# Performance work log

Hardware: AMD Instinct MI355X
Metric: run time of the kernel (lower is better)

## Reference

```python
import jax, jax.numpy as jnp
import numpy as np

N_SERIES = 1024  # N; x carries 3N stacked time-synchronous nodes
GCN_DEPTH = 2
IN_DIM = 64
H_DIM = 64


def setup_inputs() -> dict:
    key = jax.random.key(0)
    k = jax.random.split(key, 6)
    B, C, N3 = 64, IN_DIM, 3 * N_SERIES
    x = jax.random.normal(k[0], (N3, B, C), dtype=jnp.float32)
    A = jax.random.normal(k[1], (N3, N3), dtype=jnp.float32) * 0.02
    # Linear2d (1x1 conv) params per depth; act='glu' -> out = 2*h_dim
    s0 = 1.0 / np.sqrt(IN_DIM)
    s1 = 1.0 / np.sqrt(H_DIM)
    W0 = jax.random.uniform(k[2], (2 * H_DIM, IN_DIM), jnp.float32, -s0, s0)
    b0 = jax.random.uniform(k[3], (2 * H_DIM,), jnp.float32, -s0, s0)
    W1 = jax.random.uniform(k[4], (2 * H_DIM, H_DIM), jnp.float32, -s1, s1)
    b1 = jax.random.uniform(k[5], (2 * H_DIM,), jnp.float32, -s1, s1)
    return {"x": x, "A": A, "W0": W0, "b0": b0, "W1": W1, "b1": b1}


def reference(x, A, W0, b0, W1, b1):
    # x: (3N, B, C) -> (B, C, 3N)
    h = jnp.transpose(x, (1, 2, 0))
    convs = []
    for W, b in ((W0, b0), (W1, b1)):
        # GCN2d flow='tgt_to_src': h[b,c,v] = sum_w h[b,c,w] * A[v,w]  (L=1 squeezed)
        g = jnp.einsum('bcw,vw->bcv', h, A)
        # Linear2d 1x1 conv: channels C -> 2*h_dim, then GLU gate
        y = jnp.einsum('oc,bcv->bov', W, g) + b[None, :, None]
        lhs, rhs = jnp.split(y, 2, axis=1)
        h = lhs * jax.nn.sigmoid(rhs)          # (B, h_dim, 3N)
        convs.append(jnp.transpose(h, (2, 0, 1)))  # (3N, B, h_dim)
    # crop the middle N nodes of each depth, then max over depth
    cropped = jnp.stack([c[N_SERIES:2 * N_SERIES] for c in convs], axis=0)
    return jnp.max(cropped, axis=0)  # (N, B, h_dim)
```

## Files before the change

kernel.cpp:

```cpp
#include <hip/hip_runtime.h>
#include <hip/hip_bf16.h>
#include <stdint.h>

typedef __attribute__((ext_vector_type(8))) short s16x8;
typedef __attribute__((ext_vector_type(4))) float f32x4;
typedef __attribute__((ext_vector_type(8))) unsigned short u16x8;
typedef __attribute__((ext_vector_type(4))) unsigned short u16x4;

__device__ __forceinline__ float bf2f(unsigned short u) {
  union { uint32_t u; float f; } v; v.u = ((uint32_t)u) << 16; return v.f;
}
__device__ __forceinline__ unsigned short f2bf(float f) {
  union { float f; uint32_t u; } v; v.f = f;
  uint32_t u = v.u;
  return (unsigned short)((u + 0x7fffu + ((u >> 16) & 1u)) >> 16);
}
__device__ __forceinline__ void load_lds16(const void* g, void* l) {
  __builtin_amdgcn_global_load_lds(
      (const __attribute__((address_space(1))) void*)g,
      (__attribute__((address_space(3))) void*)l, 16, 0, 0);
}

template <int N>
__device__ __forceinline__ void vmw() {
  if constexpr (N == 0) asm volatile("s_waitcnt vmcnt(0)" ::: "memory");
  else if constexpr (N == 1) asm volatile("s_waitcnt vmcnt(1)" ::: "memory");
  else if constexpr (N == 2) asm volatile("s_waitcnt vmcnt(2)" ::: "memory");
  else if constexpr (N == 3) asm volatile("s_waitcnt vmcnt(3)" ::: "memory");
  else if constexpr (N == 4) asm volatile("s_waitcnt vmcnt(4)" ::: "memory");
  else if constexpr (N == 5) asm volatile("s_waitcnt vmcnt(5)" ::: "memory");
  else if constexpr (N == 6) asm volatile("s_waitcnt vmcnt(6)" ::: "memory");
  else if constexpr (N == 7) asm volatile("s_waitcnt vmcnt(7)" ::: "memory");
  else asm volatile("s_waitcnt vmcnt(8)" ::: "memory");
}
#define SBAR() asm volatile("s_barrier" ::: "memory")

__global__ __launch_bounds__(256) void k_prep(const void* __restrict__ xin,
                                              const void* __restrict__ Ain,
                                              const void* __restrict__ W0,
                                              const void* __restrict__ b0,
                                              const void* __restrict__ W1,
                                              const void* __restrict__ b1,
                                              unsigned short* __restrict__ xtp,
                                              unsigned short* __restrict__ Abp,
                                              unsigned short* __restrict__ wb) {
  __shared__ __align__(16) unsigned short sh[64 * 65];
  const int t = threadIdx.x;
  const int bid = blockIdx.x;
  int fp;
  {
    uint32_t u = ((const uint32_t*)xin)[(t & 63) * 97 + 1];
    int e = (u >> 7) & 0xFF;
    unsigned long long m = __ballot(e > 150);
    fp = (__popcll(m) > 6) ? 1 : 0;
  }

  if (bid < 3072) {
    const int w0 = (bid % 48) * 64;
    const int m0 = (bid / 48) * 64;
    if (fp) {
      const float* xf = (const float*)xin;
#pragma unroll
      for (int rep = 0; rep < 4; ++rep) {
        int vi = t + rep * 256;
        int r = vi >> 4;
        int c4 = (vi & 15) * 4;
        f32x4 v = *(const f32x4*)(xf + (uint64_t)(w0 + r) * 4096 + m0 + c4);
#pragma unroll
        for (int u = 0; u < 4; ++u) sh[(c4 + u) * 65 + r] = f2bf(v[u]);
      }
    } else {
      const unsigned short* xb = (const unsigned short*)xin;
#pragma unroll
      for (int rep = 0; rep < 2; ++rep) {
        int vi = t + rep * 256;
        int r = vi >> 3;
        int c8 = (vi & 7) * 8;
        u16x8 v = *(const u16x8*)(xb + (uint64_t)(w0 + r) * 4096 + m0 + c8);
#pragma unroll
        for (int u = 0; u < 8; ++u) sh[(c8 + u) * 65 + r] = v[u];
      }
    }
    __syncthreads();
    unsigned short* dst = xtp + ((uint64_t)(m0 >> 6) * 48 + (w0 >> 6)) * 4096;
#pragma unroll
    for (int rep = 0; rep < 2; ++rep) {
      int vi = t + rep * 256;
      int kb = vi >> 6, r = vi & 63;
      u16x8 v;
#pragma unroll
      for (int u = 0; u < 8; ++u) v[u] = sh[r * 65 + kb * 8 + u];
      *(u16x8*)(dst + kb * 512 + r * 8) = v;
    }
  } else if (bid < 5376) {
    const int b2 = bid - 3072;
    const int kt = b2 % 48, rt = b2 / 48;
    if (fp) {
      const float* Af = (const float*)Ain;
#pragma unroll
      for (int rep = 0; rep < 4; ++rep) {
        int vi = t + rep * 256;
        int r = vi >> 4;
        int c4 = (vi & 15) * 4;
        f32x4 v = *(const f32x4*)(Af + (uint64_t)(rt * 64 + r) * 3072 + kt * 64 + c4);
        int kb = c4 >> 3, e = c4 & 7;
#pragma unroll
        for (int u = 0; u < 4; ++u) sh[kb * 520 + r * 8 + e + u] = f2bf(v[u]);
      }
    } else {
      const unsigned short* Ab16 = (const unsigned short*)Ain;
#pragma unroll
      for (int rep = 0; rep < 2; ++rep) {
        int vi = t + rep * 256;
        int r = vi >> 3;
        int c8 = (vi & 7) * 8;
        u16x8 v = *(const u16x8*)(Ab16 + (uint64_t)(rt * 64 + r) * 3072 + kt * 64 + c8);
#pragma unroll
        for (int u = 0; u < 8; ++u) sh[(c8 >> 3) * 520 + r * 8 + u] = v[u];
      }
    }
    __syncthreads();
    unsigned short* dst = Abp + ((uint64_t)rt * 48 + kt) * 4096;
#pragma unroll
    for (int rep = 0; rep < 2; ++rep) {
      int vi = t + rep * 256;
      int kb = vi >> 6, r = vi & 63;
      u16x8 v;
#pragma unroll
      for (int u = 0; u < 8; ++u) v[u] = sh[kb * 520 + r * 8 + u];
      *(u16x8*)(dst + kb * 512 + r * 8) = v;
    }
  } else {
    for (int i = t; i < 16640; i += 256) {
      const void* src; int off;
      if (i < 8192)        { src = W0; off = i; }
      else if (i < 8320)   { src = b0; off = i - 8192; }
      else if (i < 16512)  { src = W1; off = i - 8320; }
      else                 { src = b1; off = i - 16512; }
      wb[i] = fp ? f2bf(((const float*)src)[off]) : ((const unsigned short*)src)[off];
    }
  }
}

__global__ __launch_bounds__(512, 2) void k1_gemm_glu(
    const unsigned short* __restrict__ Am,
    const unsigned short* __restrict__ Bm,
    const unsigned short* __restrict__ W,
    const unsigned short* __restrict__ bias,
    unsigned short* __restrict__ H) {
  constexpr int BM  = 192;
  constexpr int IF  = 6;
  constexpr int IPH = 3;
  constexpr int APL = 12;
  constexpr int P   = 28;
  constexpr int QF  = 3;
  constexpr int PPW = 4;
  constexpr int BUFS = P * 512;
  constexpr int NT  = 96;
  constexpr int Kt  = 48;
  constexpr int NRB = 12;
  constexpr int SME = 4 * BUFS;

  __shared__ __align__(16) unsigned short smem[SME];

  const int t    = threadIdx.x;
  const int lane = t & 63;
  const int wid  = t >> 6;
  const int wV   = wid >> 2;
  const int wM   = wid & 3;
  const int fr   = lane & 15;
  const int q4   = lane >> 4;
  const int v0   = blockIdx.x * BM;
  const int m0   = blockIdx.y * 256;
  const int art0 = v0 >> 6;
  const int brt0 = m0 >> 6;

  const int myq = QF + ((wid < 4) ? 1 : 0);
  const unsigned short* srcb[PPW];
  int ldso[PPW];
#pragma unroll
  for (int q = 0; q < PPW; ++q) {
    int pi = wid + 8 * q;
    if (pi >= P) pi = P - 1;
    const int isA = pi < APL;
    const int rtl = (isA ? pi : pi - APL) >> 2;
    const int pb  = pi & 3;
    const unsigned short* base =
        isA ? (Am + (uint64_t)(art0 + rtl) * Kt * 4096)
            : (Bm + (uint64_t)(brt0 + rtl) * Kt * 4096);
    srcb[q] = base + pb * 512 + lane * 8;
    ldso[q] = pi * 512;
  }

  int aoff[IF], boff[4];
#pragma unroll
  for (int i = 0; i < IF; ++i) {
    const int row = wV * 96 + i * 16 + fr;
    aoff[i] = ((row >> 6) * 4 + q4) * 512 + (row & 63) * 8;
  }
#pragma unroll
  for (int j = 0; j < 4; ++j)
    boff[j] = (APL + wM * 4 + q4) * 512 + (j * 16 + fr) * 8;

  f32x4 acc[IF][4] = {};

#pragma unroll
  for (int pt = 0; pt < 3; ++pt)
#pragma unroll
    for (int q = 0; q < PPW; ++q)
      if (q < myq)
        load_lds16(srcb[q] + pt * 2048, smem + pt * BUFS + ldso[q]);
  if (wid < 4) { vmw<8>(); } else { vmw<6>(); }
  SBAR();

#pragma unroll 4
  for (int tt = 0; tt < NT; ++tt) {
    const unsigned short* buf = smem + (tt & 3) * BUFS;
    s16x8 bfr[4];
#pragma unroll
    for (int ph = 0; ph < 2; ++ph) {
      if (ph == 0) {
#pragma unroll
        for (int j = 0; j < 4; ++j)
          bfr[j] = *(const s16x8*)(buf + boff[j]);
      }
      s16x8 afr[IPH];
#pragma unroll
      for (int ii = 0; ii < IPH; ++ii)
        afr[ii] = *(const s16x8*)(buf + aoff[ph * IPH + ii]);
      if (tt + 3 < NT) {
        unsigned short* dst = smem + ((tt + 3) & 3) * BUFS;
#pragma unroll
        for (int q = 0; q < PPW; ++q)
          if ((q % 2) == ph && q < myq)
            load_lds16(srcb[q] + (uint64_t)(tt + 3) * 2048, dst + ldso[q]);
      }
      SBAR();
      __builtin_amdgcn_s_setprio(1);
#pragma unroll
      for (int ii = 0; ii < IPH; ++ii)
#pragma unroll
        for (int j = 0; j < 4; ++j)
          acc[ph * IPH + ii][j] = __builtin_amdgcn_mfma_f32_16x16x32_bf16(
              afr[ii], bfr[j], acc[ph * IPH + ii][j], 0, 0, 0);
      __builtin_amdgcn_s_setprio(0);
      if (ph == 1) {
        if (tt + 3 < NT) {
          if (wid < 4) { vmw<8>(); } else { vmw<6>(); }
        } else if (tt + 2 < NT) {
          if (wid < 4) { vmw<4>(); } else { vmw<3>(); }
        } else {
          vmw<0>();
        }
      }
      SBAR();
    }
  }

  __syncthreads();
  {
    const int rr = q4 * 4;
#pragma unroll
    for (int i = 0; i < IF; ++i)
#pragma unroll
      for (int j = 0; j < 4; ++j) {
        const int col = wM * 64 + j * 16 + fr;
#pragma unroll
        for (int r = 0; r < 4; ++r) {
          const int row = wV * 96 + i * 16 + rr + r;
          smem[row * 264 + col] = f2bf(acc[i][j][r]);
        }
      }
  }
  __syncthreads();

  s16x8 wf[2][8];
#pragma unroll
  for (int ksi = 0; ksi < 2; ++ksi)
#pragma unroll
    for (int j = 0; j < 8; ++j)
      wf[ksi][j] = *(const s16x8*)(W + (j * 16 + fr) * 64 + ksi * 32 + q4 * 8);
  float bj[8];
#pragma unroll
  for (int j = 0; j < 8; ++j) bj[j] = bf2f(bias[j * 16 + fr]);

#pragma unroll
  for (int rep = 0; rep < 2; ++rep) {
    const int rb = rep * 8 + wid;
    if (rb < NRB) {
#pragma unroll
      for (int bb = 0; bb < 4; ++bb) {
        f32x4 acc2[8] = {};
#pragma unroll
        for (int ksi = 0; ksi < 2; ++ksi) {
          s16x8 af = *(const s16x8*)(smem + (rb * 16 + fr) * 264 + bb * 64 +
                                     ksi * 32 + q4 * 8);
#pragma unroll
          for (int j = 0; j < 8; ++j)
            acc2[j] = __builtin_amdgcn_mfma_f32_16x16x32_bf16(af, wf[ksi][j],
                                                              acc2[j], 0, 0, 0);
        }
        const int v = v0 + rb * 16 + q4 * 4;
#pragma unroll
        for (int j = 0; j < 4; ++j) {
          u16x4 pk;
#pragma unroll
          for (int r = 0; r < 4; ++r) {
            float lhs = acc2[j][r] + bj[j];
            float rhs = acc2[j + 4][r] + bj[j + 4];
            float sg = 1.0f / (1.0f + __expf(-rhs));
            pk[r] = f2bf(lhs * sg);
          }
          const int o = j * 16 + fr;
          const int hrow = m0 + bb * 64 + o;
          *(u16x4*)(H + ((uint64_t)(hrow >> 6) * 48 + (v >> 6)) * 4096 +
                    ((v >> 3) & 7) * 512 + (hrow & 63) * 8 + (v & 7)) = pk;
        }
      }
    }
  }
}

__global__ __launch_bounds__(512, 2) void k3_gemm_glu(
    const unsigned short* __restrict__ Am,
    const unsigned short* __restrict__ Bm,
    const unsigned short* __restrict__ W,
    const unsigned short* __restrict__ bias,
    const unsigned short* __restrict__ Hprev,
    float* __restrict__ outp) {
  constexpr int IF  = 2;
  constexpr int APL = 8;
  constexpr int P   = 16;
  constexpr int PPW = 2;
  constexpr int BUFS = P * 512;
  constexpr int NT  = 96;
  constexpr int Kt  = 48;
  constexpr int SME = 4 * BUFS;

  __shared__ __align__(16) unsigned short smem[SME];

  const int t    = threadIdx.x;
  const int lane = t & 63;
  const int wid  = t >> 6;
  const int wV   = wid >> 1;
  const int wM   = wid & 1;
  const int fr   = lane & 15;
  const int q4   = lane >> 4;
  const int v0   = blockIdx.x * 128;
  const int m0   = blockIdx.y * 128;
  const int art0 = 16 + (v0 >> 6);
  const int brt0 = m0 >> 6;

  const unsigned short* srcb[PPW];
  int ldso[PPW];
#pragma unroll
  for (int q = 0; q < PPW; ++q) {
    const int pi = wid + 8 * q;
    const int isA = pi < APL;
    const int rtl = (isA ? pi : pi - APL) >> 2;
    const int pb  = pi & 3;
    const unsigned short* base =
        isA ? (Am + (uint64_t)(art0 + rtl) * Kt * 4096)
            : (Bm + (uint64_t)(brt0 + rtl) * Kt * 4096);
    srcb[q] = base + pb * 512 + lane * 8;
    ldso[q] = pi * 512;
  }

  int aoff[IF], boff[4];
#pragma unroll
  for (int i = 0; i < IF; ++i) {
    const int row = wV * 32 + i * 16 + fr;
    aoff[i] = ((row >> 6) * 4 + q4) * 512 + (row & 63) * 8;
  }
#pragma unroll
  for (int j = 0; j < 4; ++j)
    boff[j] = (APL + wM * 4 + q4) * 512 + (j * 16 + fr) * 8;

  f32x4 acc[IF][4] = {};

#pragma unroll
  for (int pt = 0; pt < 3; ++pt)
#pragma unroll
    for (int q = 0; q < PPW; ++q)
      load_lds16(srcb[q] + pt * 2048, smem + pt * BUFS + ldso[q]);
  vmw<4>();
  SBAR();

#pragma unroll 4
  for (int tt = 0; tt < NT; ++tt) {
    const unsigned short* buf = smem + (tt & 3) * BUFS;
    s16x8 bfr[4], afr[IF];
#pragma unroll
    for (int j = 0; j < 4; ++j) bfr[j] = *(const s16x8*)(buf + boff[j]);
#pragma unroll
    for (int i = 0; i < IF; ++i) afr[i] = *(const s16x8*)(buf + aoff[i]);
    if (tt + 3 < NT) {
      unsigned short* pdst = smem + ((tt + 3) & 3) * BUFS;
#pragma unroll
      for (int q = 0; q < PPW; ++q)
        load_lds16(srcb[q] + (uint64_t)(tt + 3) * 2048, pdst + ldso[q]);
    }
    __builtin_amdgcn_s_setprio(1);
#pragma unroll
    for (int i = 0; i < IF; ++i)
#pragma unroll
      for (int j = 0; j < 4; ++j)
        acc[i][j] = __builtin_amdgcn_mfma_f32_16x16x32_bf16(afr[i], bfr[j],
                                                            acc[i][j], 0, 0, 0);
    __builtin_amdgcn_s_setprio(0);
    if (tt + 3 < NT) {
      vmw<4>();
    } else if (tt + 2 < NT) {
      vmw<2>();
    } else {
      vmw<0>();
    }
    SBAR();
  }

  __syncthreads();
  {
    const int rr = q4 * 4;
#pragma unroll
    for (int i = 0; i < IF; ++i)
#pragma unroll
      for (int j = 0; j < 4; ++j) {
        const int col = wM * 64 + j * 16 + fr;
#pragma unroll
        for (int r = 0; r < 4; ++r) {
          const int row = wV * 32 + i * 16 + rr + r;
          smem[row * 136 + col] = f2bf(acc[i][j][r]);
        }
      }
  }
  __syncthreads();

  s16x8 wf[2][8];
#pragma unroll
  for (int ksi = 0; ksi < 2; ++ksi)
#pragma unroll
    for (int j = 0; j < 8; ++j)
      wf[ksi][j] = *(const s16x8*)(W + (j * 16 + fr) * 64 + ksi * 32 + q4 * 8);
  float bj[8];
#pragma unroll
  for (int j = 0; j < 8; ++j) bj[j] = bf2f(bias[j * 16 + fr]);

  {
    const int rb = wid;
#pragma unroll
    for (int bb = 0; bb < 2; ++bb) {
      f32x4 acc2[8] = {};
#pragma unroll
      for (int ksi = 0; ksi < 2; ++ksi) {
        s16x8 af = *(const s16x8*)(smem + (rb * 16 + fr) * 136 + bb * 64 +
                                   ksi * 32 + q4 * 8);
#pragma unroll
        for (int j = 0; j < 8; ++j)
          acc2[j] = __builtin_amdgcn_mfma_f32_16x16x32_bf16(af, wf[ksi][j],
                                                            acc2[j], 0, 0, 0);
      }
      const int v = v0 + rb * 16 + q4 * 4;
#pragma unroll
      for (int j = 0; j < 4; ++j) {
        const int o = j * 16 + fr;
        const int hrow = m0 + bb * 64 + o;
        const int c = 1024 + v;
        u16x4 hv = *(const u16x4*)(Hprev +
            ((uint64_t)(hrow >> 6) * 48 + (c >> 6)) * 4096 +
            ((c >> 3) & 7) * 512 + (hrow & 63) * 8 + (c & 7));
        float* op = outp + (uint64_t)v * 4096 + hrow;
#pragma unroll
        for (int r = 0; r < 4; ++r) {
          float lhs = acc2[j][r] + bj[j];
          float rhs = acc2[j + 4][r] + bj[j + 4];
          float sg = 1.0f / (1.0f + __expf(-rhs));
          op[(uint64_t)r * 4096] = fmaxf(lhs * sg, bf2f(hv[r]));
        }
      }
    }
  }
}

extern "C" void kernel_launch(void* const* d_in, const int* in_sizes, int n_in,
                              void* d_out, int out_size, void* d_ws, size_t ws_size,
                              hipStream_t stream) {
  (void)in_sizes; (void)n_in; (void)out_size; (void)ws_size;
  const void* x  = d_in[0];
  const void* A  = d_in[1];
  const void* W0 = d_in[2];
  const void* b0 = d_in[3];
  const void* W1 = d_in[4];
  const void* b1 = d_in[5];
  float* out = (float*)d_out;

  char* ws = (char*)d_ws;
  unsigned short* Xtp = (unsigned short*)(ws + 0);
  unsigned short* Abp = (unsigned short*)(ws + 25165824);
  unsigned short* Wb  = (unsigned short*)(ws + 44040192);
  unsigned short* H1p = (unsigned short*)(ws + 44105728);

  k_prep<<<5377, 256, 0, stream>>>(x, A, W0, b0, W1, b1, Xtp, Abp, Wb);
  k1_gemm_glu<<<dim3(16, 16), 512, 0, stream>>>(Abp, Xtp, Wb, Wb + 8192, H1p);
  k3_gemm_glu<<<dim3(8, 32), 512, 0, stream>>>(
      Abp, H1p, Wb + 8320, Wb + 16512, H1p, out);
}
```

Measured before the change: 265.0 us.

## Load A-operand fragments directly from global into registers, stage only B in LDS

Both GEMM kernels stop staging the A (adjacency) tile through LDS. Each wave now loads its own A fragments straight from global memory into double-buffered registers one k-step ahead. Only the B tile still goes through the async global-to-LDS ring, which cuts LDS footprint and LDS read traffic per iteration. The cost is more VGPRs, exposed global latency on A, and vmcnt accounting that now mixes register loads with LDS loads.

```diff
diff --git a/kernel.cpp b/kernel.cpp
--- a/kernel.cpp
+++ b/kernel.cpp
@@ -28,9 +28,6 @@
   else if constexpr (N == 2) asm volatile("s_waitcnt vmcnt(2)" ::: "memory");
   else if constexpr (N == 3) asm volatile("s_waitcnt vmcnt(3)" ::: "memory");
   else if constexpr (N == 4) asm volatile("s_waitcnt vmcnt(4)" ::: "memory");
-  else if constexpr (N == 5) asm volatile("s_waitcnt vmcnt(5)" ::: "memory");
-  else if constexpr (N == 6) asm volatile("s_waitcnt vmcnt(6)" ::: "memory");
-  else if constexpr (N == 7) asm volatile("s_waitcnt vmcnt(7)" ::: "memory");
   else asm volatile("s_waitcnt vmcnt(8)" ::: "memory");
 }
 #define SBAR() asm volatile("s_barrier" ::: "memory")
@@ -148,18 +145,12 @@
     const unsigned short* __restrict__ W,
     const unsigned short* __restrict__ bias,
     unsigned short* __restrict__ H) {
-  constexpr int BM  = 192;
   constexpr int IF  = 6;
-  constexpr int IPH = 3;
-  constexpr int APL = 12;
-  constexpr int P   = 28;
-  constexpr int QF  = 3;
-  constexpr int PPW = 4;
-  constexpr int BUFS = P * 512;
+  constexpr int BUFS = 16 * 512;
   constexpr int NT  = 96;
   constexpr int Kt  = 48;
   constexpr int NRB = 12;
-  constexpr int SME = 4 * BUFS;
+  constexpr int SME = 192 * 264;
 
   __shared__ __align__(16) unsigned short smem[SME];
 
@@ -170,91 +161,86 @@
   const int wM   = wid & 3;
   const int fr   = lane & 15;
   const int q4   = lane >> 4;
-  const int v0   = blockIdx.x * BM;
+  const int v0   = blockIdx.x * 192;
   const int m0   = blockIdx.y * 256;
-  const int art0 = v0 >> 6;
   const int brt0 = m0 >> 6;
 
-  const int myq = QF + ((wid < 4) ? 1 : 0);
-  const unsigned short* srcb[PPW];
-  int ldso[PPW];
-#pragma unroll
-  for (int q = 0; q < PPW; ++q) {
-    int pi = wid + 8 * q;
-    if (pi >= P) pi = P - 1;
-    const int isA = pi < APL;
-    const int rtl = (isA ? pi : pi - APL) >> 2;
-    const int pb  = pi & 3;
-    const unsigned short* base =
-        isA ? (Am + (uint64_t)(art0 + rtl) * Kt * 4096)
-            : (Bm + (uint64_t)(brt0 + rtl) * Kt * 4096);
-    srcb[q] = base + pb * 512 + lane * 8;
+  const unsigned short* srcb[2];
+  int ldso[2];
+#pragma unroll
+  for (int q = 0; q < 2; ++q) {
+    const int pi = wid + 8 * q;
+    srcb[q] = Bm + ((uint64_t)(brt0 + (pi >> 2)) * Kt) * 4096 + (pi & 3) * 512 +
+              lane * 8;
     ldso[q] = pi * 512;
   }
 
-  int aoff[IF], boff[4];
+  uint64_t aog[IF];
 #pragma unroll
   for (int i = 0; i < IF; ++i) {
-    const int row = wV * 96 + i * 16 + fr;
-    aoff[i] = ((row >> 6) * 4 + q4) * 512 + (row & 63) * 8;
-  }
+    const int g = v0 + wV * 96 + i * 16 + fr;
+    aog[i] = ((uint64_t)(g >> 6) * Kt) * 4096 + q4 * 512 + (uint64_t)(g & 63) * 8;
+  }
+
+  int boff[4];
 #pragma unroll
   for (int j = 0; j < 4; ++j)
-    boff[j] = (APL + wM * 4 + q4) * 512 + (j * 16 + fr) * 8;
+    boff[j] = (wM * 4 + q4) * 512 + (j * 16 + fr) * 8;
 
   f32x4 acc[IF][4] = {};
-
+  s16x8 aA[IF], aB[IF];
+
+#pragma unroll
+  for (int i = 0; i < IF; ++i) aA[i] = *(const s16x8*)(Am + aog[i]);
 #pragma unroll
   for (int pt = 0; pt < 3; ++pt)
 #pragma unroll
-    for (int q = 0; q < PPW; ++q)
-      if (q < myq)
-        load_lds16(srcb[q] + pt * 2048, smem + pt * BUFS + ldso[q]);
-  if (wid < 4) { vmw<8>(); } else { vmw<6>(); }
+    for (int q = 0; q < 2; ++q)
+      load_lds16(srcb[q] + pt * 2048, smem + pt * BUFS + ldso[q]);
+  vmw<4>();
   SBAR();
 
-#pragma unroll 4
-  for (int tt = 0; tt < NT; ++tt) {
+  auto tile = [&](int tt, s16x8 (&CUR)[IF], s16x8 (&NXT)[IF]) {
     const unsigned short* buf = smem + (tt & 3) * BUFS;
     s16x8 bfr[4];
-#pragma unroll
-    for (int ph = 0; ph < 2; ++ph) {
-      if (ph == 0) {
-#pragma unroll
-        for (int j = 0; j < 4; ++j)
-          bfr[j] = *(const s16x8*)(buf + boff[j]);
-      }
-      s16x8 afr[IPH];
-#pragma unroll
-      for (int ii = 0; ii < IPH; ++ii)
-        afr[ii] = *(const s16x8*)(buf + aoff[ph * IPH + ii]);
-      if (tt + 3 < NT) {
-        unsigned short* dst = smem + ((tt + 3) & 3) * BUFS;
-#pragma unroll
-        for (int q = 0; q < PPW; ++q)
-          if ((q % 2) == ph && q < myq)
-            load_lds16(srcb[q] + (uint64_t)(tt + 3) * 2048, dst + ldso[q]);
-      }
-      SBAR();
-      __builtin_amdgcn_s_setprio(1);
-#pragma unroll
-      for (int ii = 0; ii < IPH; ++ii)
-#pragma unroll
-        for (int j = 0; j < 4; ++j)
-          acc[ph * IPH + ii][j] = __builtin_amdgcn_mfma_f32_16x16x32_bf16(
-              afr[ii], bfr[j], acc[ph * IPH + ii][j], 0, 0, 0);
-      __builtin_amdgcn_s_setprio(0);
-      if (ph == 1) {
-        if (tt + 3 < NT) {
-          if (wid < 4) { vmw<8>(); } else { vmw<6>(); }
-        } else if (tt + 2 < NT) {
-          if (wid < 4) { vmw<4>(); } else { vmw<3>(); }
-        } else {
-          vmw<0>();
-        }
-      }
-      SBAR();
-    }
+    if (tt + 1 < NT) {
+#pragma unroll
+      for (int i = 0; i < IF; ++i)
+        NXT[i] = *(const s16x8*)(Am + aog[i] + (uint64_t)(tt + 1) * 2048);
+    }
+#pragma unroll
+    for (int j = 0; j < 4; ++j) bfr[j] = *(const s16x8*)(buf + boff[j]);
+    if (tt + 3 < NT)
+      load_lds16(srcb[0] + (uint64_t)(tt + 3) * 2048,
+                 smem + ((tt + 3) & 3) * BUFS + ldso[0]);
+    SBAR();
+    __builtin_amdgcn_s_setprio(1);
+#pragma unroll
+    for (int ii = 0; ii < 3; ++ii)
+#pragma unroll
+      for (int j = 0; j < 4; ++j)
+        acc[ii][j] = __builtin_amdgcn_mfma_f32_16x16x32_bf16(CUR[ii], bfr[j],
+                                                             acc[ii][j], 0, 0, 0);
+    __builtin_amdgcn_s_setprio(0);
+    SBAR();
+    if (tt + 3 < NT)
+      load_lds16(srcb[1] + (uint64_t)(tt + 3) * 2048,
+                 smem + ((tt + 3) & 3) * BUFS + ldso[1]);
+    SBAR();
+    __builtin_amdgcn_s_setprio(1);
+#pragma unroll
+    for (int ii = 3; ii < 6; ++ii)
+#pragma unroll
+      for (int j = 0; j < 4; ++j)
+        acc[ii][j] = __builtin_amdgcn_mfma_f32_16x16x32_bf16(CUR[ii], bfr[j],
+                                                             acc[ii][j], 0, 0, 0);
+    __builtin_amdgcn_s_setprio(0);
+    if (tt + 3 < NT) { vmw<2>(); } else { vmw<0>(); }
+    SBAR();
+  };
+  for (int tt = 0; tt < NT; tt += 2) {
+    tile(tt, aA, aB);
+    tile(tt + 1, aB, aA);
   }
 
   __syncthreads();
@@ -329,13 +315,10 @@
     const unsigned short* __restrict__ Hprev,
     float* __restrict__ outp) {
   constexpr int IF  = 2;
-  constexpr int APL = 8;
-  constexpr int P   = 16;
-  constexpr int PPW = 2;
-  constexpr int BUFS = P * 512;
+  constexpr int BUFS = 8 * 512;
   constexpr int NT  = 96;
   constexpr int Kt  = 48;
-  constexpr int SME = 4 * BUFS;
+  constexpr int SME = 128 * 136;
 
   __shared__ __align__(16) unsigned short smem[SME];
 
@@ -348,74 +331,63 @@
   const int q4   = lane >> 4;
   const int v0   = blockIdx.x * 128;
   const int m0   = blockIdx.y * 128;
-  const int art0 = 16 + (v0 >> 6);
   const int brt0 = m0 >> 6;
 
-  const unsigned short* srcb[PPW];
-  int ldso[PPW];
-#pragma unroll
-  for (int q = 0; q < PPW; ++q) {
-    const int pi = wid + 8 * q;
-    const int isA = pi < APL;
-    const int rtl = (isA ? pi : pi - APL) >> 2;
-    const int pb  = pi & 3;
-    const unsigned short* base =
-        isA ? (Am + (uint64_t)(art0 + rtl) * Kt * 4096)
-            : (Bm + (uint64_t)(brt0 + rtl) * Kt * 4096);
-    srcb[q] = base + pb * 512 + lane * 8;
-    ldso[q] = pi * 512;
-  }
-
-  int aoff[IF], boff[4];
+  const unsigned short* srcb0 =
+      Bm + ((uint64_t)(brt0 + (wid >> 2)) * Kt) * 4096 + (wid & 3) * 512 +
+      lane * 8;
+  const int ldso0 = wid * 512;
+
+  uint64_t aog[IF];
 #pragma unroll
   for (int i = 0; i < IF; ++i) {
-    const int row = wV * 32 + i * 16 + fr;
-    aoff[i] = ((row >> 6) * 4 + q4) * 512 + (row & 63) * 8;
-  }
+    const int g = 1024 + v0 + wV * 32 + i * 16 + fr;
+    aog[i] = ((uint64_t)(g >> 6) * Kt) * 4096 + q4 * 512 + (uint64_t)(g & 63) * 8;
+  }
+
+  int boff[4];
 #pragma unroll
   for (int j = 0; j < 4; ++j)
-    boff[j] = (APL + wM * 4 + q4) * 512 + (j * 16 + fr) * 8;
+    boff[j] = (wM * 4 + q4) * 512 + (j * 16 + fr) * 8;
 
   f32x4 acc[IF][4] = {};
-
+  s16x8 aA[IF], aB[IF];
+
+#pragma unroll
+  for (int i = 0; i < IF; ++i) aA[i] = *(const s16x8*)(Am + aog[i]);
 #pragma unroll
   for (int pt = 0; pt < 3; ++pt)
-#pragma unroll
-    for (int q = 0; q < PPW; ++q)
-      load_lds16(srcb[q] + pt * 2048, smem + pt * BUFS + ldso[q]);
-  vmw<4>();
+    load_lds16(srcb0 + pt * 2048, smem + pt * BUFS + ldso0);
+  vmw<2>();
   SBAR();
 
-#pragma unroll 4
-  for (int tt = 0; tt < NT; ++tt) {
+  auto tile = [&](int tt, s16x8 (&CUR)[IF], s16x8 (&NXT)[IF]) {
     const unsigned short* buf = smem + (tt & 3) * BUFS;
-    s16x8 bfr[4], afr[IF];
+    s16x8 bfr[4];
+    if (tt + 1 < NT) {
+#pragma unroll
+      for (int i = 0; i < IF; ++i)
+        NXT[i] = *(const s16x8*)(Am + aog[i] + (uint64_t)(tt + 1) * 2048);
+    }
 #pragma unroll
     for (int j = 0; j < 4; ++j) bfr[j] = *(const s16x8*)(buf + boff[j]);
-#pragma unroll
-    for (int i = 0; i < IF; ++i) afr[i] = *(const s16x8*)(buf + aoff[i]);
-    if (tt + 3 < NT) {
-      unsigned short* pdst = smem + ((tt + 3) & 3) * BUFS;
-#pragma unroll
-      for (int q = 0; q < PPW; ++q)
-        load_lds16(srcb[q] + (uint64_t)(tt + 3) * 2048, pdst + ldso[q]);
-    }
+    if (tt + 3 < NT)
+      load_lds16(srcb0 + (uint64_t)(tt + 3) * 2048,
+                 smem + ((tt + 3) & 3) * BUFS + ldso0);
     __builtin_amdgcn_s_setprio(1);
 #pragma unroll
     for (int i = 0; i < IF; ++i)
 #pragma unroll
       for (int j = 0; j < 4; ++j)
-        acc[i][j] = __builtin_amdgcn_mfma_f32_16x16x32_bf16(afr[i], bfr[j],
+        acc[i][j] = __builtin_amdgcn_mfma_f32_16x16x32_bf16(CUR[i], bfr[j],
                                                             acc[i][j], 0, 0, 0);
     __builtin_amdgcn_s_setprio(0);
-    if (tt + 3 < NT) {
-      vmw<4>();
-    } else if (tt + 2 < NT) {
-      vmw<2>();
-    } else {
-      vmw<0>();
-    }
+    if (tt + 3 < NT) { vmw<1>(); } else { vmw<0>(); }
     SBAR();
+  };
+  for (int tt = 0; tt < NT; tt += 2) {
+    tile(tt, aA, aB);
+    tile(tt + 1, aB, aA);
   }
 
   __syncthreads();
```

After: 321.8 us. 21.4% more time.
